# Kernel optimization log

Measured on AMD Instinct MI355X. Metric: run time of the kernel, lower is better.

Reference implementation:

```python
import jax, jax.numpy as jnp
import numpy as np

BATCH = 65536
DIM = 512
NUM_CLASSES = 1000
NUM_OLD = 500  # old_classes == set(range(NUM_OLD))


def setup_inputs() -> dict:
    key = jax.random.key(0)
    k1, k2, k3 = jax.random.split(key, 3)
    embeddings = jax.random.normal(k1, (BATCH, DIM), dtype=jnp.float32)
    centroids = jax.random.normal(k2, (NUM_CLASSES, DIM), dtype=jnp.float32)
    labels = jax.random.randint(k3, (BATCH,), 0, NUM_CLASSES, dtype=jnp.int64 if jax.config.jax_enable_x64 else jnp.int32)
    return {"embeddings": embeddings, "centroids": centroids, "labels": labels, "num_old": NUM_OLD}


def reference(embeddings, centroids, labels, num_old):
    # Fused gather + per-sample MSE + masked mean (replaces the per-sample Python loop).
    gathered = centroids[labels]                                  # [B, D]
    per_sample = jnp.mean((embeddings - gathered) ** 2, axis=-1)  # [B], F.mse_loss per sample
    # Original accumulates dis.detach(): the loss value carries no gradient.
    per_sample = jax.lax.stop_gradient(per_sample)
    mask = labels < num_old                                       # label in old_classes
    count = jnp.sum(mask)
    total = jnp.sum(jnp.where(mask, per_sample, jnp.float32(0.0)))
    # if count == 0: return raw (zero) loss, else mean
    loss = jnp.where(count == 0, total, total / jnp.maximum(count, 1).astype(total.dtype))
    return loss
```

## Files before the change

### kernel.cpp

```cpp
#include <hip/hip_runtime.h>

constexpr int kDim = 512;
constexpr int kF4PerRow = kDim / 4;

__device__ __forceinline__ float sqdiff4(float4 e, float4 c) {
    float d, t;
    d = e.x - c.x; t  = d * d;
    d = e.y - c.y; t += d * d;
    d = e.z - c.z; t += d * d;
    d = e.w - c.w; t += d * d;
    return t;
}

__global__ __launch_bounds__(256) void mse_masked_kernel(
    const float* __restrict__ emb,
    const float* __restrict__ cen,
    const int* __restrict__ labels,
    const int* __restrict__ num_old_p,
    int batch,
    float* __restrict__ ws_sum,
    unsigned int* __restrict__ ws_cnt)
{
    const int num_old = *num_old_p;
    const int lane = threadIdx.x & 63;
    const int wid  = threadIdx.x >> 6;
    const int wpb  = blockDim.x >> 6;
    const int gwave = blockIdx.x * wpb + wid;
    const int nwave = gridDim.x * wpb;

    const int half = gwave & 1;
    const int col  = half * 64 + lane;

    const float4* __restrict__ emb4 = (const float4*)emb;
    const float4* __restrict__ cen4 = (const float4*)cen;

    float acc = 0.0f;
    unsigned int cnt = 0;

    const int nchunks = (batch + 63) >> 6;
    for (int ch = (gwave >> 1); ch < nchunks; ch += (nwave >> 1)) {
        const int chunk = ch * 64;
        const int idx = chunk + lane;
        const int mylab = (idx < batch) ? labels[idx] : 0x7fffffff;
        unsigned long long m = __ballot(mylab < num_old);
        if (half == 0) cnt += (unsigned int)__popcll(m);

        while (__popcll(m) >= 8) {
            int b[8], l[8];
            #pragma unroll
            for (int i = 0; i < 8; ++i) { b[i] = __builtin_ctzll(m); m &= m - 1; }
            #pragma unroll
            for (int i = 0; i < 8; ++i) l[i] = __shfl(mylab, b[i], 64);

            float4 e[8], c[8];
            #pragma unroll
            for (int i = 0; i < 8; ++i)
                e[i] = emb4[(size_t)(chunk + b[i]) * kF4PerRow + col];
            #pragma unroll
            for (int i = 0; i < 8; ++i)
                c[i] = cen4[(size_t)l[i] * kF4PerRow + col];

            #pragma unroll
            for (int i = 0; i < 8; ++i)
                acc += sqdiff4(e[i], c[i]);
        }
        while (m) {
            const int b = __builtin_ctzll(m); m &= m - 1;
            const int l = __shfl(mylab, b, 64);
            float4 e = emb4[(size_t)(chunk + b) * kF4PerRow + col];
            float4 c = cen4[(size_t)l * kF4PerRow + col];
            acc += sqdiff4(e, c);
        }
    }

    #pragma unroll
    for (int off = 32; off > 0; off >>= 1)
        acc += __shfl_xor(acc, off, 64);

    __shared__ float        s_sum[8];
    __shared__ unsigned int s_cnt[8];
    if (lane == 0) { s_sum[wid] = acc; s_cnt[wid] = cnt; }
    __syncthreads();

    if (threadIdx.x == 0) {
        float        bs = 0.0f;
        unsigned int bc = 0u;
        for (int i = 0; i < wpb; ++i) { bs += s_sum[i]; bc += s_cnt[i]; }
        ws_sum[blockIdx.x] = bs;
        ws_cnt[blockIdx.x] = bc;
    }
}

__global__ __launch_bounds__(256) void finalize_kernel(
    const float* __restrict__ ws_sum,
    const unsigned int* __restrict__ ws_cnt,
    int nparts,
    float* __restrict__ out)
{
    const int t = threadIdx.x;
    float        s = 0.0f;
    unsigned int c = 0u;
    for (int i = t; i < nparts; i += blockDim.x) { s += ws_sum[i]; c += ws_cnt[i]; }

    #pragma unroll
    for (int off = 32; off > 0; off >>= 1) {
        s += __shfl_xor(s, off, 64);
        c += __shfl_xor(c, off, 64);
    }
    __shared__ float        ls[4];
    __shared__ unsigned int lc[4];
    const int lane = t & 63, wid = t >> 6;
    if (lane == 0) { ls[wid] = s; lc[wid] = c; }
    __syncthreads();
    if (t == 0) {
        float        ts = ls[0] + ls[1] + ls[2] + ls[3];
        unsigned int tc = lc[0] + lc[1] + lc[2] + lc[3];
        const float total = ts * (1.0f / (float)kDim);
        out[0] = (tc == 0u) ? total : total / (float)tc;
    }
}

extern "C" void kernel_launch(void* const* d_in, const int* in_sizes, int n_in,
                              void* d_out, int out_size, void* d_ws, size_t ws_size,
                              hipStream_t stream) {
    const float* emb       = (const float*)d_in[0];
    const float* cen       = (const float*)d_in[1];
    const int*   labels    = (const int*)d_in[2];
    const int*   num_old_p = (const int*)d_in[3];

    const int batch = in_sizes[2];

    const int blocks = 512;
    float*        ws_sum = (float*)d_ws;
    unsigned int* ws_cnt = (unsigned int*)((char*)d_ws + blocks * sizeof(float));

    mse_masked_kernel<<<blocks, 256, 0, stream>>>(emb, cen, labels, num_old_p,
                                                  batch, ws_sum, ws_cnt);
    finalize_kernel<<<1, 256, 0, stream>>>(ws_sum, ws_cnt, blocks, (float*)d_out);
}
```

Before: 187.0 us.

## Fuse finalize into main kernel via cooperative grid sync; use nontemporal embedding loads

Replaces the separate finalize kernel with a cooperative launch in which all blocks write partials, synchronize with a grid-wide barrier, and block 0 performs the final reduction. This removes one kernel launch. It also loads embeddings with nontemporal hints so the streamed data is less likely to evict the reused centroid rows from cache. The grid barrier adds its own cost, and cooperative launch requires all 512 blocks to be co-resident.

```diff
diff --git a/kernel.cpp b/kernel.cpp
--- a/kernel.cpp
+++ b/kernel.cpp
@@ -1,25 +1,29 @@
 #include <hip/hip_runtime.h>
+#include <hip/hip_cooperative_groups.h>
+
+namespace cg = cooperative_groups;
 
 constexpr int kDim = 512;
 constexpr int kF4PerRow = kDim / 4;
+constexpr int kBlocks = 512;
 
-__device__ __forceinline__ float sqdiff4(float4 e, float4 c) {
-    float d, t;
-    d = e.x - c.x; t  = d * d;
-    d = e.y - c.y; t += d * d;
-    d = e.z - c.z; t += d * d;
-    d = e.w - c.w; t += d * d;
-    return t;
+typedef float f32x4 __attribute__((ext_vector_type(4)));
+
+__device__ __forceinline__ float sqdiff4(f32x4 e, f32x4 c) {
+    f32x4 d = e - c;
+    d = d * d;
+    return d.x + d.y + d.z + d.w;
 }
 
-__global__ __launch_bounds__(256) void mse_masked_kernel(
+__global__ __launch_bounds__(256) void mse_fused_kernel(
     const float* __restrict__ emb,
     const float* __restrict__ cen,
     const int* __restrict__ labels,
     const int* __restrict__ num_old_p,
     int batch,
     float* __restrict__ ws_sum,
-    unsigned int* __restrict__ ws_cnt)
+    unsigned int* __restrict__ ws_cnt,
+    float* __restrict__ out)
 {
     const int num_old = *num_old_p;
     const int lane = threadIdx.x & 63;
@@ -31,8 +35,8 @@
     const int half = gwave & 1;
     const int col  = half * 64 + lane;
 
-    const float4* __restrict__ emb4 = (const float4*)emb;
-    const float4* __restrict__ cen4 = (const float4*)cen;
+    const f32x4* __restrict__ emb4 = (const f32x4*)emb;
+    const f32x4* __restrict__ cen4 = (const f32x4*)cen;
 
     float acc = 0.0f;
     unsigned int cnt = 0;
@@ -52,10 +56,10 @@
             #pragma unroll
             for (int i = 0; i < 8; ++i) l[i] = __shfl(mylab, b[i], 64);
 
-            float4 e[8], c[8];
+            f32x4 e[8], c[8];
             #pragma unroll
             for (int i = 0; i < 8; ++i)
-                e[i] = emb4[(size_t)(chunk + b[i]) * kF4PerRow + col];
+                e[i] = __builtin_nontemporal_load(&emb4[(size_t)(chunk + b[i]) * kF4PerRow + col]);
             #pragma unroll
             for (int i = 0; i < 8; ++i)
                 c[i] = cen4[(size_t)l[i] * kF4PerRow + col];
@@ -67,8 +71,8 @@
         while (m) {
             const int b = __builtin_ctzll(m); m &= m - 1;
             const int l = __shfl(mylab, b, 64);
-            float4 e = emb4[(size_t)(chunk + b) * kF4PerRow + col];
-            float4 c = cen4[(size_t)l * kF4PerRow + col];
+            f32x4 e = __builtin_nontemporal_load(&emb4[(size_t)(chunk + b) * kF4PerRow + col]);
+            f32x4 c = cen4[(size_t)l * kF4PerRow + col];
             acc += sqdiff4(e, c);
         }
     }
@@ -77,8 +81,8 @@
     for (int off = 32; off > 0; off >>= 1)
         acc += __shfl_xor(acc, off, 64);
 
-    __shared__ float        s_sum[8];
-    __shared__ unsigned int s_cnt[8];
+    __shared__ float        s_sum[4];
+    __shared__ unsigned int s_cnt[4];
     if (lane == 0) { s_sum[wid] = acc; s_cnt[wid] = cnt; }
     __syncthreads();
 
@@ -89,34 +93,31 @@
         ws_sum[blockIdx.x] = bs;
         ws_cnt[blockIdx.x] = bc;
     }
-}
+    __threadfence();
 
-__global__ __launch_bounds__(256) void finalize_kernel(
-    const float* __restrict__ ws_sum,
-    const unsigned int* __restrict__ ws_cnt,
-    int nparts,
-    float* __restrict__ out)
-{
-    const int t = threadIdx.x;
-    float        s = 0.0f;
-    unsigned int c = 0u;
-    for (int i = t; i < nparts; i += blockDim.x) { s += ws_sum[i]; c += ws_cnt[i]; }
+    cg::this_grid().sync();
 
-    #pragma unroll
-    for (int off = 32; off > 0; off >>= 1) {
-        s += __shfl_xor(s, off, 64);
-        c += __shfl_xor(c, off, 64);
-    }
-    __shared__ float        ls[4];
-    __shared__ unsigned int lc[4];
-    const int lane = t & 63, wid = t >> 6;
-    if (lane == 0) { ls[wid] = s; lc[wid] = c; }
-    __syncthreads();
-    if (t == 0) {
-        float        ts = ls[0] + ls[1] + ls[2] + ls[3];
-        unsigned int tc = lc[0] + lc[1] + lc[2] + lc[3];
-        const float total = ts * (1.0f / (float)kDim);
-        out[0] = (tc == 0u) ? total : total / (float)tc;
+    if (blockIdx.x == 0) {
+        const int t = threadIdx.x;
+        float        s = 0.0f;
+        unsigned int c = 0u;
+        for (int i = t; i < kBlocks; i += blockDim.x) { s += ws_sum[i]; c += ws_cnt[i]; }
+
+        #pragma unroll
+        for (int off = 32; off > 0; off >>= 1) {
+            s += __shfl_xor(s, off, 64);
+            c += __shfl_xor(c, off, 64);
+        }
+        __shared__ float        ls[4];
+        __shared__ unsigned int lc[4];
+        if (lane == 0) { ls[wid] = s; lc[wid] = c; }
+        __syncthreads();
+        if (t == 0) {
+            float        ts = ls[0] + ls[1] + ls[2] + ls[3];
+            unsigned int tc = lc[0] + lc[1] + lc[2] + lc[3];
+            const float total = ts * (1.0f / (float)kDim);
+            out[0] = (tc == 0u) ? total : total / (float)tc;
+        }
     }
 }
 
@@ -127,14 +128,14 @@
     const float* cen       = (const float*)d_in[1];
     const int*   labels    = (const int*)d_in[2];
     const int*   num_old_p = (const int*)d_in[3];
+    int batch = in_sizes[2];
 
-    const int batch = in_sizes[2];
+    float*        ws_sum = (float*)d_ws;
+    unsigned int* ws_cnt = (unsigned int*)((char*)d_ws + kBlocks * sizeof(float));
+    float*        out    = (float*)d_out;
 
-    const int blocks = 512;
-    float*        ws_sum = (float*)d_ws;
-    unsigned int* ws_cnt = (unsigned int*)((char*)d_ws + blocks * sizeof(float));
-
-    mse_masked_kernel<<<blocks, 256, 0, stream>>>(emb, cen, labels, num_old_p,
-                                                  batch, ws_sum, ws_cnt);
-    finalize_kernel<<<1, 256, 0, stream>>>(ws_sum, ws_cnt, blocks, (float*)d_out);
+    void* args[] = { (void*)&emb, (void*)&cen, (void*)&labels, (void*)&num_old_p,
+                     (void*)&batch, (void*)&ws_sum, (void*)&ws_cnt, (void*)&out };
+    (void)hipLaunchCooperativeKernel((const void*)mse_fused_kernel,
+                                     dim3(kBlocks), dim3(256), args, 0, stream);
 }
```

Result: slower. 290.1 us (+55.1%).
